# Optimization experiments

Measured on AMD Instinct MI355X. Metric: run time of the kernel, lower is better.

## Reference

```python
import jax, jax.numpy as jnp
import numpy as np

B, T, DM, H, DK, DV = 2, 2048, 1024, 16, 64, 64


def setup_inputs() -> dict:
    key = jax.random.key(0)
    k = jax.random.split(key, 7)
    std_k = np.float32(1.0 / np.sqrt(DK))
    std_v = np.float32(1.0 / np.sqrt(DV))
    return {
        "xq": jax.random.normal(k[0], (B, T, DM), jnp.float32),
        "xk": jax.random.normal(k[1], (B, T, DM), jnp.float32),
        "xv": jax.random.normal(k[2], (B, T, DM), jnp.float32),
        "mask": jnp.ones((B, T), jnp.float32),  # padding mask: 1 = keep
        "w_q": jax.random.normal(k[3], (H, DM, DK), jnp.float32) * std_k,
        "w_k": jax.random.normal(k[4], (H, DM, DK), jnp.float32) * std_k,
        "w_v": jax.random.normal(k[5], (H, DM, DV), jnp.float32) * std_v,
        "w_o": jax.random.normal(k[6], (H * DV, DM), jnp.float32) * np.float32(1.0 / np.sqrt(H * DV)),
        "b_o": jnp.zeros((DM,), jnp.float32),
    }


def reference(xq, xk, xv, mask, w_q, w_k, w_v, w_o, b_o):
    d_k = w_q.shape[-1]
    # per-head projections: [B,T,DM] x [H,DM,DK] -> [B,H,T,DK]
    q = jnp.einsum('bsd,hdk->bhsk', xq, w_q)
    kk = jnp.einsum('btd,hdk->bhtk', xk, w_k)
    v = jnp.einsum('btd,hdv->bhtv', xv, w_v)
    # NOTE: source divides by d_k (not sqrt(d_k)) -- kept faithful
    scores = jnp.einsum('bhsk,bhtk->bhst', q, kk) / jnp.float32(d_k)
    # _padding_mask: multiply by mask broadcast over key dim, then any exact
    # zero (masked OR coincidentally zero score) becomes -inf -- kept faithful
    masked = scores * mask[:, None, None, :]
    scores = jnp.where(masked == 0.0, -jnp.inf, masked)
    attn = jax.nn.softmax(scores, axis=-1)
    out = jnp.einsum('bhst,bhtv->bhsv', attn, v)  # [B,H,T,DV]
    b, h, t, dv = out.shape
    concat = out.transpose(0, 2, 1, 3).reshape(b, t, h * dv)
    return concat @ w_o + b_o
```

## Files before the change

kernel.cpp:

```cpp
#include <hip/hip_runtime.h>
#include <hip/hip_bf16.h>


typedef __attribute__((ext_vector_type(8))) short short8;
typedef __attribute__((ext_vector_type(4))) short short4v;
typedef __attribute__((ext_vector_type(4))) float f32x4;
typedef __attribute__((ext_vector_type(4))) int i32x4;

__device__ __forceinline__ short f2bf(float f) {
  union { float f; unsigned u; } v; v.f = f;
  unsigned r = v.u + 0x7FFFu + ((v.u >> 16) & 1u);
  return (short)(r >> 16);
}

#define GLD_LDS(g, l) __builtin_amdgcn_global_load_lds( \
    (const __attribute__((address_space(1))) void*)(g), \
    (__attribute__((address_space(3))) void*)(l), 16, 0, 0)

__global__ __launch_bounds__(256) void prep_all(
    const float* __restrict__ xq, const float* __restrict__ xk,
    const float* __restrict__ xv, const float* __restrict__ wq,
    const float* __restrict__ wk, const float* __restrict__ wv,
    const float* __restrict__ wo,
    short* __restrict__ Xb, short* __restrict__ Wall, short* __restrict__ Wot)
{
  const int bx = blockIdx.x, tid = threadIdx.x;
  __shared__ float Lt[64][65];
  if (bx < 6144) {
    int z = bx >> 11;
    const float* x = z == 0 ? xq : (z == 1 ? xk : xv);
    size_t i = ((size_t)(bx & 2047) * 256 + tid) * 8;
    f32x4 f0 = *(const f32x4*)(x + i);
    f32x4 f1 = *(const f32x4*)(x + i + 4);
    short8 s;
#pragma unroll
    for (int j = 0; j < 4; j++) { s[j] = f2bf(f0[j]); s[4 + j] = f2bf(f1[j]); }
    *(short8*)(Xb + (size_t)z * 4194304 + i) = s;
  } else if (bx < 6912) {
    int bz = bx - 6144;
    int z = bz >> 8, inner = bz & 255;
    const float* w = z == 0 ? wq : (z == 1 ? wk : wv);
    short* Wt = Wall + (size_t)z * 1048576;
    int h = inner >> 4, d0 = (inner & 15) * 64;
#pragma unroll
    for (int it = 0; it < 4; it++) {
      int e = tid + it * 256;
      int dl = e >> 4, k4 = (e & 15) * 4;
      f32x4 v = *(const f32x4*)(w + ((size_t)(h * 1024 + d0 + dl) * 64) + k4);
#pragma unroll
      for (int j = 0; j < 4; j++) Lt[dl][k4 + j] = v[j];
    }
    __syncthreads();
#pragma unroll
    for (int it = 0; it < 4; it++) {
      int e = tid + it * 256;
      int kl = e >> 4, dq = e & 15;
      short4v s;
#pragma unroll
      for (int j = 0; j < 4; j++) s[j] = f2bf(Lt[dq * 4 + j][kl]);
      *(short4v*)(Wt + (size_t)(h * 64 + kl) * 1024 + d0 + dq * 4) = s;
    }
  } else {
    int bz = bx - 6912;
    int k0 = (bz >> 4) * 64, n0 = (bz & 15) * 64;
#pragma unroll
    for (int it = 0; it < 4; it++) {
      int e = tid + it * 256;
      int kl = e >> 4, n4 = (e & 15) * 4;
      f32x4 v = *(const f32x4*)(wo + (size_t)(k0 + kl) * 1024 + n0 + n4);
#pragma unroll
      for (int j = 0; j < 4; j++) Lt[kl][n4 + j] = v[j];
    }
    __syncthreads();
#pragma unroll
    for (int it = 0; it < 4; it++) {
      int e = tid + it * 256;
      int nl = e >> 4, kq = e & 15;
      short4v s;
#pragma unroll
      for (int j = 0; j < 4; j++) s[j] = f2bf(Lt[kq * 4 + j][nl]);
      *(short4v*)(Wot + (size_t)(n0 + nl) * 1024 + k0 + kq * 4) = s;
    }
  }
}

__global__ __launch_bounds__(256) void proj_qkv2(
    const short* __restrict__ Xb, const short* __restrict__ Wall,
    short* __restrict__ Qb, short* __restrict__ Kt2, short* __restrict__ Vt2)
{
  const int z = blockIdx.z;
  const short* X  = Xb   + (size_t)z * 4194304;
  const short* Wt = Wall + (size_t)z * 1048576;

  const int t0 = blockIdx.x * 128;
  const int n0 = blockIdx.y * 128;
  const int tid = threadIdx.x, w = tid >> 6, lane = tid & 63;
  const int c = lane & 15, q4 = lane >> 4;
  const int wn = (w & 1) * 64, wt = (w >> 1) * 64;
  const int srow = lane >> 2, scol = (lane & 3) * 8;

  __shared__ __align__(16) short Al[128 * 32];
  __shared__ __align__(16) short Bl[128 * 32];

  f32x4 acc[4][4] = {};

  for (int k0 = 0; k0 < 1024; k0 += 32) {
#pragma unroll
    for (int i = 0; i < 2; i++) {
      int rg = (w * 2 + i) * 16;
      GLD_LDS(Wt + (size_t)(n0 + rg + srow) * 1024 + k0 + scol, Al + rg * 32);
      GLD_LDS(X  + (size_t)(t0 + rg + srow) * 1024 + k0 + scol, Bl + rg * 32);
    }
    __syncthreads();
    short8 a[4], bfr[4];
#pragma unroll
    for (int i = 0; i < 4; i++)
      a[i] = *(const short8*)(Al + (wn + i * 16 + c) * 32 + q4 * 8);
#pragma unroll
    for (int j = 0; j < 4; j++)
      bfr[j] = *(const short8*)(Bl + (wt + j * 16 + c) * 32 + q4 * 8);
#pragma unroll
    for (int i = 0; i < 4; i++)
#pragma unroll
      for (int j = 0; j < 4; j++)
        acc[i][j] = __builtin_amdgcn_mfma_f32_16x16x32_bf16(a[i], bfr[j], acc[i][j], 0, 0, 0);
    __syncthreads();
  }

#pragma unroll
  for (int i = 0; i < 4; i++)
#pragma unroll
    for (int j = 0; j < 4; j++) {
      int n = n0 + wn + i * 16 + q4 * 4;
      int trow = t0 + wt + j * 16 + c;
      int b = trow >> 11, t = trow & 2047;
      int h = n >> 6, cc = n & 63;
      int bh = b * 16 + h;
      f32x4 v = acc[i][j];
      short4v pk;
#pragma unroll
      for (int r = 0; r < 4; r++) pk[r] = f2bf(v[r]);
      if (z == 0) {
        *(short4v*)(Qb + (size_t)(bh * 2048 + t) * 64 + cc) = pk;
      } else if (z == 1) {
        int t5 = t & 31, s_ = t5 >> 4, c_ = t5 & 15;
        size_t base = (size_t)bh * 131072 + (t >> 5) * 2048;
#pragma unroll
        for (int r = 0; r < 4; r++) {
          int dv = cc + r;
          Kt2[base + ((s_ * 2 + (dv >> 5)) * 16 + c_) * 32 + ((dv >> 3) & 3) * 8 + (dv & 7)] = pk[r];
        }
      } else {
        int t5 = t & 31;
        int kp = ((t5 >> 2) & 3) * 8 + ((t5 >> 4) & 1) * 4 + (t5 & 3);
        size_t base = (size_t)bh * 131072 + (t >> 5) * 2048;
#pragma unroll
        for (int r = 0; r < 4; r++)
          Vt2[base + (size_t)(cc + r) * 32 + kp] = pk[r];
      }
    }
}

__global__ __launch_bounds__(256, 2) void attn7(
    const short* __restrict__ Qb, const short* __restrict__ Kt2,
    const short* __restrict__ Vt2, const float* __restrict__ mask,
    short* __restrict__ AO)
{
  const int tblk = blockIdx.x;
  const int bh = blockIdx.y;
  const int b = bh >> 4, h = bh & 15;
  const short* Qh = Qb  + (size_t)bh * 131072;
  const short* Kh = Kt2 + (size_t)bh * 131072;
  const short* Vh = Vt2 + (size_t)bh * 131072;

  const int tid = threadIdx.x, w = tid >> 6, lane = tid & 63;
  const int c = lane & 15, q4 = lane >> 4;
  const int qrow0 = tblk * 128 + w * 32;

  __shared__ __align__(16) short KV[2][4096];

  const int ch = c * 4 + q4;
  const int rdo = (ch ^ ((ch >> 3) & 3)) * 8;
  const int sch = (lane ^ ((lane >> 3) & 3)) * 8;

  short8 qa[2][2];
#pragma unroll
  for (int u = 0; u < 2; u++)
#pragma unroll
    for (int dc = 0; dc < 2; dc++)
      qa[u][dc] = *(const short8*)(Qh + (size_t)(qrow0 + u * 16 + c) * 64 + dc * 32 + q4 * 8);

  f32x4 acc[2][4] = {};
  float l[2] = {0.f, 0.f};
  const float LOG2E_64 = 1.44269504088896f * 0.015625f;
  const float* mP = mask + b * 2048 + q4 * 4;

  const int g0 = w * 2;

#define STAGE(BUF, T) do { \
    const short* sb = (g0 < 4) ? (Kh + (size_t)(T) * 2048 + g0 * 512) \
                               : (Vh + (size_t)(T) * 2048 + (g0 - 4) * 512); \
    GLD_LDS(sb + sch,        &KV[BUF][g0 * 512]); \
    GLD_LDS(sb + 512 + sch,  &KV[BUF][g0 * 512 + 512]); \
  } while (0)

#define BODY(BUF) do { \
    short8 kf[2][2], va[4]; \
    _Pragma("unroll") \
    for (int s = 0; s < 2; s++) \
      _Pragma("unroll") \
      for (int dc = 0; dc < 2; dc++) \
        kf[s][dc] = *(const short8*)(&KV[BUF][(s * 2 + dc) * 512 + rdo]); \
    _Pragma("unroll") \
    for (int vs = 0; vs < 4; vs++) \
      va[vs] = *(const short8*)(&KV[BUF][(4 + vs) * 512 + rdo]); \
    f32x4 st[2][2] = {}; \
    _Pragma("unroll") \
    for (int u = 0; u < 2; u++) \
      _Pragma("unroll") \
      for (int s = 0; s < 2; s++) { \
        st[u][s] = __builtin_amdgcn_mfma_f32_16x16x32_bf16(kf[s][0], qa[u][0], st[u][s], 0, 0, 0); \
        st[u][s] = __builtin_amdgcn_mfma_f32_16x16x32_bf16(kf[s][1], qa[u][1], st[u][s], 0, 0, 0); \
      } \
    f32x4 cm[2], cb[2]; \
    _Pragma("unroll") \
    for (int s = 0; s < 2; s++) { \
      f32x4 mk = *(const f32x4*)(mP + s * 16); \
      cm[s] = mk * LOG2E_64; \
      cb[s] = (mk - 1.0f) * 240.0f; \
    } \
    mP += 32; \
    _Pragma("unroll") \
    for (int u = 0; u < 2; u++) { \
      unsigned pkd[2][2]; \
      _Pragma("unroll") \
      for (int s = 0; s < 2; s++) { \
        float e0 = __builtin_amdgcn_exp2f(st[u][s][0] * cm[s][0] + cb[s][0]); \
        float e1 = __builtin_amdgcn_exp2f(st[u][s][1] * cm[s][1] + cb[s][1]); \
        float e2 = __builtin_amdgcn_exp2f(st[u][s][2] * cm[s][2] + cb[s][2]); \
        float e3 = __builtin_amdgcn_exp2f(st[u][s][3] * cm[s][3] + cb[s][3]); \
        l[u] += (e0 + e1) + (e2 + e3); \
        union { float f; unsigned u; } a0, a1, a2, a3; \
        a0.f = e0; a1.f = e1; a2.f = e2; a3.f = e3; \
        pkd[s][0] = __builtin_amdgcn_perm(a1.u + 0x8000u, a0.u + 0x8000u, 0x07060302u); \
        pkd[s][1] = __builtin_amdgcn_perm(a3.u + 0x8000u, a2.u + 0x8000u, 0x07060302u); \
      } \
      union { i32x4 i; short8 s; } pb; \
      pb.i[0] = (int)pkd[0][0]; pb.i[1] = (int)pkd[0][1]; \
      pb.i[2] = (int)pkd[1][0]; pb.i[3] = (int)pkd[1][1]; \
      _Pragma("unroll") \
      for (int vs = 0; vs < 4; vs++) \
        acc[u][vs] = __builtin_amdgcn_mfma_f32_16x16x32_bf16(va[vs], pb.s, acc[u][vs], 0, 0, 0); \
    } \
  } while (0)

  STAGE(0, 0);
  asm volatile("s_waitcnt vmcnt(0)" ::: "memory");
  __syncthreads();
  int cur = 0;
  for (int t = 0; t < 63; ++t) {
    STAGE(cur ^ 1, t + 1);
    BODY(cur);
    asm volatile("s_waitcnt vmcnt(0)" ::: "memory");
    __syncthreads();
    cur ^= 1;
  }
  BODY(cur);
#undef STAGE
#undef BODY

#pragma unroll
  for (int u = 0; u < 2; u++) {
    float lu = l[u];
    lu += __shfl_xor(lu, 16);
    lu += __shfl_xor(lu, 32);
    float inv = 1.0f / lu;
    size_t row = (size_t)b * 2048 + qrow0 + u * 16 + c;
#pragma unroll
    for (int vs = 0; vs < 4; vs++) {
      f32x4 v = acc[u][vs];
      short4v pk;
#pragma unroll
      for (int r = 0; r < 4; r++) pk[r] = f2bf(v[r] * inv);
      *(short4v*)(AO + row * 1024 + h * 64 + vs * 16 + q4 * 4) = pk;
    }
  }
}

__global__ __launch_bounds__(256) void out_proj2(
    const short* __restrict__ AO, const short* __restrict__ Wot,
    const float* __restrict__ bo, float* __restrict__ out)
{
  const int t0 = blockIdx.x * 128;
  const int n0 = blockIdx.y * 128;
  const int tid = threadIdx.x, w = tid >> 6, lane = tid & 63;
  const int c = lane & 15, q4 = lane >> 4;
  const int wn = (w & 1) * 64, wt = (w >> 1) * 64;
  const int srow = lane >> 2, scol = (lane & 3) * 8;

  __shared__ __align__(16) short Al[128 * 32];
  __shared__ __align__(16) short Bl[128 * 32];

  f32x4 acc[4][4] = {};

  for (int k0 = 0; k0 < 1024; k0 += 32) {
#pragma unroll
    for (int i = 0; i < 2; i++) {
      int rg = (w * 2 + i) * 16;
      GLD_LDS(Wot + (size_t)(n0 + rg + srow) * 1024 + k0 + scol, Al + rg * 32);
      GLD_LDS(AO  + (size_t)(t0 + rg + srow) * 1024 + k0 + scol, Bl + rg * 32);
    }
    __syncthreads();
    short8 a[4], bfr[4];
#pragma unroll
    for (int i = 0; i < 4; i++)
      a[i] = *(const short8*)(Al + (wn + i * 16 + c) * 32 + q4 * 8);
#pragma unroll
    for (int j = 0; j < 4; j++)
      bfr[j] = *(const short8*)(Bl + (wt + j * 16 + c) * 32 + q4 * 8);
#pragma unroll
    for (int i = 0; i < 4; i++)
#pragma unroll
      for (int j = 0; j < 4; j++)
        acc[i][j] = __builtin_amdgcn_mfma_f32_16x16x32_bf16(a[i], bfr[j], acc[i][j], 0, 0, 0);
    __syncthreads();
  }

#pragma unroll
  for (int i = 0; i < 4; i++)
#pragma unroll
    for (int j = 0; j < 4; j++) {
      int n = n0 + wn + i * 16 + q4 * 4;
      int trow = t0 + wt + j * 16 + c;
      f32x4 v = acc[i][j] + *(const f32x4*)(bo + n);
      *(f32x4*)(out + (size_t)trow * 1024 + n) = v;
    }
}

extern "C" void kernel_launch(void* const* d_in, const int* in_sizes, int n_in,
                              void* d_out, int out_size, void* d_ws, size_t ws_size,
                              hipStream_t stream)
{
  (void)in_sizes; (void)n_in; (void)out_size; (void)ws_size;
  const float* xq   = (const float*)d_in[0];
  const float* xk   = (const float*)d_in[1];
  const float* xv   = (const float*)d_in[2];
  const float* mask = (const float*)d_in[3];
  const float* wq   = (const float*)d_in[4];
  const float* wk   = (const float*)d_in[5];
  const float* wv   = (const float*)d_in[6];
  const float* wo   = (const float*)d_in[7];
  const float* bo   = (const float*)d_in[8];
  float* out = (float*)d_out;

  char* ws = (char*)d_ws;
  short* Wall = (short*)(ws + (size_t)0);
  short* Wot  = (short*)(ws + ((size_t)6 << 20));
  short* Xb   = (short*)(ws + ((size_t)8 << 20));
  short* AO   = (short*)(ws + ((size_t)8 << 20));
  short* Qb   = (short*)(ws + ((size_t)32 << 20));
  short* Kt2  = (short*)(ws + ((size_t)40 << 20));
  short* Vt2  = (short*)(ws + ((size_t)48 << 20));

  prep_all<<<7168, 256, 0, stream>>>(xq, xk, xv, wq, wk, wv, wo, Xb, Wall, Wot);
  proj_qkv2<<<dim3(32, 8, 3), 256, 0, stream>>>(Xb, Wall, Qb, Kt2, Vt2);
  attn7<<<dim3(16, 32), 256, 0, stream>>>(Qb, Kt2, Vt2, mask, AO);
  out_proj2<<<dim3(32, 8), 256, 0, stream>>>(AO, Wot, bo, out);
}
```

Measured before the change: 228.3 us.

## Triple-buffer K/V tiles in attention and stage padding mask in LDS

The attention kernel moves from a double-buffered to a triple-buffered K/V LDS ring. Loads are issued two tiles ahead, and each iteration waits only on the older load with vmcnt(2) plus a single barrier, instead of fully draining memory and syncing after every tile. The per-batch padding mask is copied into LDS once, so each tile no longer issues a global mask load. The grid axes are also swapped so consecutive blocks walk across heads. The cost is more LDS per block, which could affect occupancy at two blocks per CU.

Measured after the change: 224.5 us. No clear change (-1.7%).

```diff
diff --git a/kernel.cpp b/kernel.cpp
--- a/kernel.cpp
+++ b/kernel.cpp
@@ -161,13 +161,13 @@
     }
 }
 
-__global__ __launch_bounds__(256, 2) void attn7(
+__global__ __launch_bounds__(256, 2) void attn8(
     const short* __restrict__ Qb, const short* __restrict__ Kt2,
     const short* __restrict__ Vt2, const float* __restrict__ mask,
     short* __restrict__ AO)
 {
-  const int tblk = blockIdx.x;
-  const int bh = blockIdx.y;
+  const int bh = blockIdx.x;
+  const int tblk = blockIdx.y;
   const int b = bh >> 4, h = bh & 15;
   const short* Qh = Qb  + (size_t)bh * 131072;
   const short* Kh = Kt2 + (size_t)bh * 131072;
@@ -177,12 +177,20 @@
   const int c = lane & 15, q4 = lane >> 4;
   const int qrow0 = tblk * 128 + w * 32;
 
-  __shared__ __align__(16) short KV[2][4096];
+  __shared__ __align__(16) short KV[3][4096];
+  __shared__ __align__(16) float Ml[2048];
 
   const int ch = c * 4 + q4;
   const int rdo = (ch ^ ((ch >> 3) & 3)) * 8;
   const int sch = (lane ^ ((lane >> 3) & 3)) * 8;
 
+  {
+    f32x4 m0 = *(const f32x4*)(mask + b * 2048 + tid * 8);
+    f32x4 m1 = *(const f32x4*)(mask + b * 2048 + tid * 8 + 4);
+    *(f32x4*)(&Ml[tid * 8]) = m0;
+    *(f32x4*)(&Ml[tid * 8 + 4]) = m1;
+  }
+
   short8 qa[2][2];
 #pragma unroll
   for (int u = 0; u < 2; u++)
@@ -193,27 +201,27 @@
   f32x4 acc[2][4] = {};
   float l[2] = {0.f, 0.f};
   const float LOG2E_64 = 1.44269504088896f * 0.015625f;
-  const float* mP = mask + b * 2048 + q4 * 4;
 
   const int g0 = w * 2;
 
-#define STAGE(BUF, T) do { \
+#define STAGE(BI, T) do { \
     const short* sb = (g0 < 4) ? (Kh + (size_t)(T) * 2048 + g0 * 512) \
                                : (Vh + (size_t)(T) * 2048 + (g0 - 4) * 512); \
-    GLD_LDS(sb + sch,        &KV[BUF][g0 * 512]); \
-    GLD_LDS(sb + 512 + sch,  &KV[BUF][g0 * 512 + 512]); \
+    GLD_LDS(sb + sch,        &KV[BI][g0 * 512]); \
+    GLD_LDS(sb + 512 + sch,  &KV[BI][g0 * 512 + 512]); \
   } while (0)
 
-#define BODY(BUF) do { \
+#define BODY(BI, TT) do { \
+    const short* Kb = &KV[BI][0]; \
     short8 kf[2][2], va[4]; \
     _Pragma("unroll") \
     for (int s = 0; s < 2; s++) \
       _Pragma("unroll") \
       for (int dc = 0; dc < 2; dc++) \
-        kf[s][dc] = *(const short8*)(&KV[BUF][(s * 2 + dc) * 512 + rdo]); \
+        kf[s][dc] = *(const short8*)(Kb + (s * 2 + dc) * 512 + rdo); \
     _Pragma("unroll") \
     for (int vs = 0; vs < 4; vs++) \
-      va[vs] = *(const short8*)(&KV[BUF][(4 + vs) * 512 + rdo]); \
+      va[vs] = *(const short8*)(Kb + (4 + vs) * 512 + rdo); \
     f32x4 st[2][2] = {}; \
     _Pragma("unroll") \
     for (int u = 0; u < 2; u++) \
@@ -225,11 +233,10 @@
     f32x4 cm[2], cb[2]; \
     _Pragma("unroll") \
     for (int s = 0; s < 2; s++) { \
-      f32x4 mk = *(const f32x4*)(mP + s * 16); \
+      f32x4 mk = *(const f32x4*)(&Ml[(TT) * 32 + q4 * 4 + s * 16]); \
       cm[s] = mk * LOG2E_64; \
       cb[s] = (mk - 1.0f) * 240.0f; \
     } \
-    mP += 32; \
     _Pragma("unroll") \
     for (int u = 0; u < 2; u++) { \
       unsigned pkd[2][2]; \
@@ -254,18 +261,33 @@
     } \
   } while (0)
 
+  __syncthreads();
+  asm volatile("s_waitcnt vmcnt(0)" ::: "memory");
+  __builtin_amdgcn_sched_barrier(0);
   STAGE(0, 0);
+  STAGE(1, 1);
+
+  int bi = 0;
+  for (int t = 0; t < 62; ++t) {
+    asm volatile("s_waitcnt vmcnt(2)" ::: "memory");
+    __builtin_amdgcn_sched_barrier(0);
+    __builtin_amdgcn_s_barrier();
+    __builtin_amdgcn_sched_barrier(0);
+    int si = bi + 2; if (si >= 3) si -= 3;
+    STAGE(si, t + 2);
+    BODY(bi, t);
+    bi = (bi + 1 == 3) ? 0 : bi + 1;
+  }
+  asm volatile("s_waitcnt vmcnt(2)" ::: "memory");
+  __builtin_amdgcn_sched_barrier(0);
+  __builtin_amdgcn_s_barrier();
+  __builtin_amdgcn_sched_barrier(0);
+  BODY(bi, 62);
   asm volatile("s_waitcnt vmcnt(0)" ::: "memory");
-  __syncthreads();
-  int cur = 0;
-  for (int t = 0; t < 63; ++t) {
-    STAGE(cur ^ 1, t + 1);
-    BODY(cur);
-    asm volatile("s_waitcnt vmcnt(0)" ::: "memory");
-    __syncthreads();
-    cur ^= 1;
-  }
-  BODY(cur);
+  __builtin_amdgcn_sched_barrier(0);
+  __builtin_amdgcn_s_barrier();
+  __builtin_amdgcn_sched_barrier(0);
+  BODY(0, 63);
 #undef STAGE
 #undef BODY
 
@@ -364,6 +386,6 @@
 
   prep_all<<<7168, 256, 0, stream>>>(xq, xk, xv, wq, wk, wv, wo, Xb, Wall, Wot);
   proj_qkv2<<<dim3(32, 8, 3), 256, 0, stream>>>(Xb, Wall, Qb, Kt2, Vt2);
-  attn7<<<dim3(16, 32), 256, 0, stream>>>(Qb, Kt2, Vt2, mask, AO);
+  attn8<<<dim3(32, 16), 256, 0, stream>>>(Qb, Kt2, Vt2, mask, AO);
   out_proj2<<<dim3(32, 8), 256, 0, stream>>>(AO, Wot, bo, out);
 }
```

## Double K/V tile per sync in attention, precompute mask factors in LDS

Applied to the files above, without the earlier changes.

The attention kernel now stages two 32-key K/V tiles per pipeline step, halving the number of barriers and wait points, and precomputes the mask scale and bias into LDS once per block instead of loading them from global memory every iteration. It also swaps the grid order so blocks of the same head are adjacent, replaces the manual bf16 packing with v_cvt_pk_bf16_f32, and writes K projections with a single vector store instead of four scalar stores. The costs are more LDS per block (32KB for K/V plus 16KB of mask tables), which may limit occupancy, and a different rounding mode for the probability packing.

After: 220.4 us. -3.5%, faster.

```diff
diff --git a/kernel.cpp b/kernel.cpp
--- a/kernel.cpp
+++ b/kernel.cpp
@@ -145,11 +145,9 @@
       } else if (z == 1) {
         int t5 = t & 31, s_ = t5 >> 4, c_ = t5 & 15;
         size_t base = (size_t)bh * 131072 + (t >> 5) * 2048;
-#pragma unroll
-        for (int r = 0; r < 4; r++) {
-          int dv = cc + r;
-          Kt2[base + ((s_ * 2 + (dv >> 5)) * 16 + c_) * 32 + ((dv >> 3) & 3) * 8 + (dv & 7)] = pk[r];
-        }
+        size_t off = base + ((s_ * 2 + (cc >> 5)) * 16 + c_) * 32 +
+                     ((cc >> 3) & 3) * 8 + (cc & 7);
+        *(short4v*)(Kt2 + off) = pk;
       } else {
         int t5 = t & 31;
         int kp = ((t5 >> 2) & 3) * 8 + ((t5 >> 4) & 1) * 4 + (t5 & 3);
@@ -161,13 +159,13 @@
     }
 }
 
-__global__ __launch_bounds__(256, 2) void attn7(
+__global__ __launch_bounds__(256, 2) void attn14(
     const short* __restrict__ Qb, const short* __restrict__ Kt2,
     const short* __restrict__ Vt2, const float* __restrict__ mask,
     short* __restrict__ AO)
 {
-  const int tblk = blockIdx.x;
-  const int bh = blockIdx.y;
+  const int bh = blockIdx.x;
+  const int tblk = blockIdx.y;
   const int b = bh >> 4, h = bh & 15;
   const short* Qh = Qb  + (size_t)bh * 131072;
   const short* Kh = Kt2 + (size_t)bh * 131072;
@@ -177,12 +175,24 @@
   const int c = lane & 15, q4 = lane >> 4;
   const int qrow0 = tblk * 128 + w * 32;
 
-  __shared__ __align__(16) short KV[2][4096];
+  __shared__ __align__(16) short KV2[2][8192];
+  __shared__ __align__(16) float cmL[2048];
+  __shared__ __align__(16) float cbL[2048];
 
   const int ch = c * 4 + q4;
   const int rdo = (ch ^ ((ch >> 3) & 3)) * 8;
   const int sch = (lane ^ ((lane >> 3) & 3)) * 8;
 
+  {
+    const float LOG2E_64c = 1.44269504088896f * 0.015625f;
+    f32x4 m0 = *(const f32x4*)(mask + b * 2048 + tid * 8);
+    f32x4 m1 = *(const f32x4*)(mask + b * 2048 + tid * 8 + 4);
+    *(f32x4*)(&cmL[tid * 8])     = m0 * LOG2E_64c;
+    *(f32x4*)(&cmL[tid * 8 + 4]) = m1 * LOG2E_64c;
+    *(f32x4*)(&cbL[tid * 8])     = (m0 - 1.0f) * 240.0f;
+    *(f32x4*)(&cbL[tid * 8 + 4]) = (m1 - 1.0f) * 240.0f;
+  }
+
   short8 qa[2][2];
 #pragma unroll
   for (int u = 0; u < 2; u++)
@@ -192,44 +202,46 @@
 
   f32x4 acc[2][4] = {};
   float l[2] = {0.f, 0.f};
-  const float LOG2E_64 = 1.44269504088896f * 0.015625f;
-  const float* mP = mask + b * 2048 + q4 * 4;
 
   const int g0 = w * 2;
 
-#define STAGE(BUF, T) do { \
-    const short* sb = (g0 < 4) ? (Kh + (size_t)(T) * 2048 + g0 * 512) \
-                               : (Vh + (size_t)(T) * 2048 + (g0 - 4) * 512); \
-    GLD_LDS(sb + sch,        &KV[BUF][g0 * 512]); \
-    GLD_LDS(sb + 512 + sch,  &KV[BUF][g0 * 512 + 512]); \
+#define STAGE(BI, P) do { \
+    const short* s0 = (g0 < 4) ? (Kh + (size_t)(2 * (P)) * 2048 + g0 * 512) \
+                               : (Vh + (size_t)(2 * (P)) * 2048 + (g0 - 4) * 512); \
+    GLD_LDS(s0 + sch,         &KV2[BI][g0 * 512]); \
+    GLD_LDS(s0 + 512 + sch,   &KV2[BI][g0 * 512 + 512]); \
+    const short* s1 = (g0 < 4) ? (Kh + (size_t)(2 * (P) + 1) * 2048 + g0 * 512) \
+                               : (Vh + (size_t)(2 * (P) + 1) * 2048 + (g0 - 4) * 512); \
+    GLD_LDS(s1 + sch,         &KV2[BI][4096 + g0 * 512]); \
+    GLD_LDS(s1 + 512 + sch,   &KV2[BI][4096 + g0 * 512 + 512]); \
   } while (0)
 
-#define BODY(BUF) do { \
+#define BODY1(KB, TT) do { \
+    const short* Kb = (KB); \
     short8 kf[2][2], va[4]; \
     _Pragma("unroll") \
     for (int s = 0; s < 2; s++) \
       _Pragma("unroll") \
       for (int dc = 0; dc < 2; dc++) \
-        kf[s][dc] = *(const short8*)(&KV[BUF][(s * 2 + dc) * 512 + rdo]); \
+        kf[s][dc] = *(const short8*)(Kb + (s * 2 + dc) * 512 + rdo); \
     _Pragma("unroll") \
     for (int vs = 0; vs < 4; vs++) \
-      va[vs] = *(const short8*)(&KV[BUF][(4 + vs) * 512 + rdo]); \
-    f32x4 st[2][2] = {}; \
+      va[vs] = *(const short8*)(Kb + 2048 + vs * 512 + rdo); \
+    f32x4 st[2][2]; \
     _Pragma("unroll") \
     for (int u = 0; u < 2; u++) \
       _Pragma("unroll") \
       for (int s = 0; s < 2; s++) { \
-        st[u][s] = __builtin_amdgcn_mfma_f32_16x16x32_bf16(kf[s][0], qa[u][0], st[u][s], 0, 0, 0); \
-        st[u][s] = __builtin_amdgcn_mfma_f32_16x16x32_bf16(kf[s][1], qa[u][1], st[u][s], 0, 0, 0); \
+        f32x4 z = {}; \
+        z = __builtin_amdgcn_mfma_f32_16x16x32_bf16(kf[s][0], qa[u][0], z, 0, 0, 0); \
+        st[u][s] = __builtin_amdgcn_mfma_f32_16x16x32_bf16(kf[s][1], qa[u][1], z, 0, 0, 0); \
       } \
     f32x4 cm[2], cb[2]; \
     _Pragma("unroll") \
     for (int s = 0; s < 2; s++) { \
-      f32x4 mk = *(const f32x4*)(mP + s * 16); \
-      cm[s] = mk * LOG2E_64; \
-      cb[s] = (mk - 1.0f) * 240.0f; \
+      cm[s] = *(const f32x4*)(&cmL[(TT) * 32 + q4 * 4 + s * 16]); \
+      cb[s] = *(const f32x4*)(&cbL[(TT) * 32 + q4 * 4 + s * 16]); \
     } \
-    mP += 32; \
     _Pragma("unroll") \
     for (int u = 0; u < 2; u++) { \
       unsigned pkd[2][2]; \
@@ -240,10 +252,10 @@
         float e2 = __builtin_amdgcn_exp2f(st[u][s][2] * cm[s][2] + cb[s][2]); \
         float e3 = __builtin_amdgcn_exp2f(st[u][s][3] * cm[s][3] + cb[s][3]); \
         l[u] += (e0 + e1) + (e2 + e3); \
-        union { float f; unsigned u; } a0, a1, a2, a3; \
-        a0.f = e0; a1.f = e1; a2.f = e2; a3.f = e3; \
-        pkd[s][0] = __builtin_amdgcn_perm(a1.u + 0x8000u, a0.u + 0x8000u, 0x07060302u); \
-        pkd[s][1] = __builtin_amdgcn_perm(a3.u + 0x8000u, a2.u + 0x8000u, 0x07060302u); \
+        unsigned p01, p23; \
+        asm("v_cvt_pk_bf16_f32 %0, %1, %2" : "=v"(p01) : "v"(e0), "v"(e1)); \
+        asm("v_cvt_pk_bf16_f32 %0, %1, %2" : "=v"(p23) : "v"(e2), "v"(e3)); \
+        pkd[s][0] = p01; pkd[s][1] = p23; \
       } \
       union { i32x4 i; short8 s; } pb; \
       pb.i[0] = (int)pkd[0][0]; pb.i[1] = (int)pkd[0][1]; \
@@ -254,19 +266,27 @@
     } \
   } while (0)
 
+#define BODY(BI, P) do { \
+    BODY1(&KV2[BI][0],    2 * (P)); \
+    BODY1(&KV2[BI][4096], 2 * (P) + 1); \
+  } while (0)
+
+  __syncthreads();
+  asm volatile("s_waitcnt vmcnt(0)" ::: "memory");
   STAGE(0, 0);
   asm volatile("s_waitcnt vmcnt(0)" ::: "memory");
   __syncthreads();
   int cur = 0;
-  for (int t = 0; t < 63; ++t) {
-    STAGE(cur ^ 1, t + 1);
-    BODY(cur);
+  for (int p = 0; p < 31; ++p) {
+    STAGE(cur ^ 1, p + 1);
+    BODY(cur, p);
     asm volatile("s_waitcnt vmcnt(0)" ::: "memory");
     __syncthreads();
     cur ^= 1;
   }
-  BODY(cur);
+  BODY(cur, 31);
 #undef STAGE
+#undef BODY1
 #undef BODY
 
 #pragma unroll
@@ -364,6 +384,6 @@
 
   prep_all<<<7168, 256, 0, stream>>>(xq, xk, xv, wq, wk, wv, wo, Xb, Wall, Wot);
   proj_qkv2<<<dim3(32, 8, 3), 256, 0, stream>>>(Xb, Wall, Qb, Kt2, Vt2);
-  attn7<<<dim3(16, 32), 256, 0, stream>>>(Qb, Kt2, Vt2, mask, AO);
+  attn14<<<dim3(32, 16), 256, 0, stream>>>(Qb, Kt2, Vt2, mask, AO);
   out_proj2<<<dim3(32, 8), 256, 0, stream>>>(AO, Wot, bo, out);
 }
```
